# Performance work log

Hardware: AMD Instinct MI355X
Metric: run time of the kernel (lower is better)

## Reference

```python
import jax, jax.numpy as jnp
import numpy as np

TRNA_N, DIS_N = 8000, 6000
D, H, E, B = 128, 256, 320000, 16384
NEG_SLOPE = 0.2  # gat_alpha
TEMP = 0.5


def _gat(src, tgt, s_idx, t_idx, Wsrc, Wtgt, a, n_src):
    # BipartiteGraphAttentionLayer (eval mode, dropout off)
    h_i = src @ Wsrc.T            # [n_src, D]
    h_j = tgt @ Wtgt.T            # [n_tgt, D]
    # cat([h_i[s], h_j[t]]) @ a == (h_i @ a[:D])[s] + (h_j @ a[D:])[t]
    s_i = h_i @ a[:D]             # [n_src]
    s_j = h_j @ a[D:]             # [n_tgt]
    e = jax.nn.leaky_relu(s_i[s_idx] + s_j[t_idx], NEG_SLOPE)
    e = jnp.clip(e, -30.0, 30.0)
    exp_e = jnp.exp(e)
    denom = jax.ops.segment_sum(exp_e, s_idx, num_segments=n_src)
    alpha = exp_e / (denom[s_idx] + 1e-8)
    out = jax.ops.segment_sum(h_j[t_idx] * alpha[:, None], s_idx, num_segments=n_src)
    return jax.nn.elu(out)


def _hg(x, S):
    # HCCF-style parameter-free hypergraph conv: nodes -> hyperedges -> nodes
    return jax.nn.elu(S @ (S.T @ x))


def _info_nce(z1, z2):
    z1 = z1 / (jnp.linalg.norm(z1, axis=1, keepdims=True) + 1e-12)
    z2 = z2 / (jnp.linalg.norm(z2, axis=1, keepdims=True) + 1e-12)
    sim = (z1 @ z2.T) / TEMP      # [N, N]
    logp = jax.nn.log_softmax(sim, axis=1)
    return -jnp.mean(jnp.diagonal(logp))


def setup_inputs():
    key = jax.random.key(0)
    ks = jax.random.split(key, 20)
    xn = lambda k, shp, sc: jax.random.normal(k, shp, dtype=jnp.float32) * sc
    d2 = (2.0 / (2 * D)) ** 0.5
    return dict(
        trna_embed=xn(ks[0], (TRNA_N, D), (2.0 / (TRNA_N + D)) ** 0.5),
        disease_embed=xn(ks[1], (DIS_N, D), (2.0 / (DIS_N + D)) ** 0.5),
        thyper=xn(ks[2], (D, H), (2.0 / (D + H)) ** 0.5),
        dhyper=xn(ks[3], (D, H), (2.0 / (D + H)) ** 0.5),
        gat_t_Wsrc=xn(ks[4], (3, D, D), d2),
        gat_t_Wtgt=xn(ks[5], (3, D, D), d2),
        gat_t_a=xn(ks[6], (3, 2 * D), 1.414 * (2.0 / (2 * D + 1)) ** 0.5),
        gat_d_Wsrc=xn(ks[7], (3, D, D), d2),
        gat_d_Wtgt=xn(ks[8], (3, D, D), d2),
        gat_d_a=xn(ks[9], (3, 2 * D), 1.414 * (2.0 / (2 * D + 1)) ** 0.5),
        mlp_W1=xn(ks[10], (D, 2 * D), (2.0 / (3 * D)) ** 0.5),
        mlp_b1=jnp.zeros((D,), jnp.float32),
        mlp_W2=xn(ks[11], (1, D), (2.0 / (D + 1)) ** 0.5),
        mlp_b2=jnp.zeros((1,), jnp.float32),
        gate_W=xn(ks[12], (1, D), (2.0 / (D + 1)) ** 0.5),
        gate_b=jnp.zeros((1,), jnp.float32),
        src_id=jax.random.randint(ks[13], (E,), 0, TRNA_N),
        tgt_id=jax.random.randint(ks[14], (E,), 0, DIS_N),
        trna_ids=jax.random.randint(ks[15], (B,), 0, TRNA_N),
        disease_ids=jax.random.randint(ks[16], (B,), 0, DIS_N),
    )


def reference(trna_embed, disease_embed, thyper, dhyper,
              gat_t_Wsrc, gat_t_Wtgt, gat_t_a,
              gat_d_Wsrc, gat_d_Wtgt, gat_d_a,
              mlp_W1, mlp_b1, mlp_W2, mlp_b2, gate_W, gate_b,
              src_id, tgt_id, trna_ids, disease_ids):
    # stage 1: simple-graph GAT pass
    sg_t = _gat(trna_embed, disease_embed, src_id, tgt_id,
                gat_t_Wsrc[0], gat_t_Wtgt[0], gat_t_a[0], TRNA_N)
    sg_d = _gat(disease_embed, sg_t, tgt_id, src_id,
                gat_d_Wsrc[0], gat_d_Wtgt[0], gat_d_a[0], DIS_N)
    # hypergraph passes 1-2
    hg_t = _hg(sg_t, sg_t @ thyper)
    hg_d = _hg(sg_d, sg_d @ dhyper)
    hg_t = _hg(hg_t, hg_t @ thyper)
    hg_d = _hg(hg_d, hg_d @ dhyper)
    # GAT layers 2-3 on hypergraph outputs
    sg_t = _gat(hg_t, hg_d, src_id, tgt_id,
                gat_t_Wsrc[1], gat_t_Wtgt[1], gat_t_a[1], TRNA_N)
    sg_d = _gat(hg_d, hg_t, tgt_id, src_id,
                gat_d_Wsrc[1], gat_d_Wtgt[1], gat_d_a[1], DIS_N)
    sg_t = _gat(sg_t, sg_d, src_id, tgt_id,
                gat_t_Wsrc[2], gat_t_Wtgt[2], gat_t_a[2], TRNA_N)
    sg_d = _gat(sg_d, sg_t, tgt_id, src_id,
                gat_d_Wsrc[2], gat_d_Wtgt[2], gat_d_a[2], DIS_N)
    # hypergraph pass 3
    hg_t = _hg(hg_t, hg_t @ thyper)
    hg_d = _hg(hg_d, hg_d @ dhyper)
    final_t = sg_t + hg_t
    final_d = sg_d + hg_d
    sel_t = final_t[trna_ids]
    sel_d = final_d[disease_ids]
    contrast = _info_nce(sg_t, hg_t) + _info_nce(sg_d, hg_d)
    gmf_vec = sel_t * sel_d
    gmf_pred = jnp.sum(gmf_vec, axis=-1)
    mlp_in = jnp.concatenate([sel_t, sel_d], axis=-1)
    h1 = jax.nn.relu(mlp_in @ mlp_W1.T + mlp_b1)
    mlp_pred = (h1 @ mlp_W2.T + mlp_b2)[:, 0]
    gate = jax.nn.sigmoid(gmf_vec @ gate_W.T + gate_b)[:, 0]
    fusion_pred = gate * gmf_pred + (1.0 - gate) * mlp_pred
    return (fusion_pred, sg_t, sg_d, gmf_pred, mlp_pred, contrast)
```

## Files before the change

### kernel.cpp

```cpp
#include <hip/hip_runtime.h>
#include <math.h>

#define N_T 8000
#define N_D 6000
#define N_E 320000
#define N_B 16384
#define NSTRIP 12

typedef __attribute__((ext_vector_type(8))) short s16x8;
typedef __attribute__((ext_vector_type(8))) __bf16 bf16x8;
typedef __attribute__((ext_vector_type(4))) float f32x4;

static __device__ __forceinline__ f32x4 mfma16(s16x8 a, s16x8 b, f32x4 c) {
  return __builtin_amdgcn_mfma_f32_16x16x32_bf16(
      __builtin_bit_cast(bf16x8, a), __builtin_bit_cast(bf16x8, b), c, 0, 0, 0);
}

static __device__ __forceinline__ unsigned short f2bf(float f) {
  unsigned u = __float_as_uint(f);
  u += 0x7FFF + ((u >> 16) & 1);
  return (unsigned short)(u >> 16);
}

static __device__ __forceinline__ float bf2f(unsigned short u) {
// ... 42 lines not shown
    int incl = buf[threadIdx.x];
    if (i < n) { int e = c0 + incl - v; rp[i] = e; cur[i] = e; }
    __syncthreads();
    if (threadIdx.x == 0) carry_s = c0 + buf[1023];
    __syncthreads();
  }
  if (threadIdx.x == 0) rp[n] = carry_s;
}

__global__ void k_scatter2(const int* __restrict__ src, const int* __restrict__ tgt,
    int* __restrict__ cur_t, int* __restrict__ cur_d,
    int* __restrict__ nbr_t, int* __restrict__ nbr_d) {
  int i = blockIdx.x * 256 + threadIdx.x;
  if (i < N_E) {
    int p = atomicAdd(&cur_t[src[i]], 1);
    nbr_t[p] = tgt[i];
  } else if (i < 2 * N_E) {
    i -= N_E;
    int p = atomicAdd(&cur_d[tgt[i]], 1);
    nbr_d[p] = src[i];
  }
}

__global__ __launch_bounds__(256) void k_pgemm(const float* __restrict__ th,
    const float* __restrict__ dh, float* __restrict__ P_t, float* __restrict__ P_d) {
  const float* A = blockIdx.x < 4 ? th : dh;
  float* C = blockIdx.x < 4 ? P_t : P_d;
  const int sub = blockIdx.x & 3;
  const int row0 = (sub >> 1) * 64, col0 = (sub & 1) * 64;
  __shared__ float As[16][65];
  __shared__ float Bs[16][65];
  const int tid = threadIdx.x;
  const int tr = tid >> 4, tc = tid & 15;
  float acc[4][4] = {};
  for (int k0 = 0; k0 < 256; k0 += 16) {
    {
      int m = tid >> 2, kk = (tid & 3) * 4;
      float4 v = *(const float4*)(A + (size_t)(row0 + m) * 256 + k0 + kk);
      As[kk + 0][m] = v.x; As[kk + 1][m] = v.y; As[kk + 2][m] = v.z; As[kk + 3][m] = v.w;
    }
    {
      int nn = tid >> 2, kk = (tid & 3) * 4;
      float4 v = *(const float4*)(A + (size_t)(col0 + nn) * 256 + k0 + kk);
      Bs[kk + 0][nn] = v.x; Bs[kk + 1][nn] = v.y; Bs[kk + 2][nn] = v.z; Bs[kk + 3][nn] = v.w;
    }
    __syncthreads();
#pragma unroll
    for (int k = 0; k < 16; ++k) {
      float a[4], b[4];
#pragma unroll
      for (int i = 0; i < 4; ++i) a[i] = As[k][tr * 4 + i];
#pragma unroll
      for (int j = 0; j < 4; ++j) b[j] = Bs[k][tc * 4 + j];
#pragma unroll
      for (int i = 0; i < 4; ++i)
#pragma unroll
        for (int j = 0; j < 4; ++j)
          acc[i][j] = fmaf(a[i], b[j], acc[i][j]);
    }
    __syncthreads();
  }
#pragma unroll
  for (int i = 0; i < 4; ++i)
#pragma unroll
    for (int j = 0; j < 4; ++j)
      C[(size_t)(row0 + tr * 4 + i) * 128 + col0 + tc * 4 + j] = acc[i][j];
}

__global__ void k_tobf16m(const float* __restrict__ a0, unsigned short* __restrict__ y0,
    const float* __restrict__ a1, unsigned short* __restrict__ y1,
    const float* __restrict__ a2, unsigned short* __restrict__ y2,
    const float* __restrict__ a3, unsigned short* __restrict__ y3) {
  int i = blockIdx.x * 256 + threadIdx.x;
  const float* x; unsigned short* y;
  if (i < 12288) { x = a0; y = y0; }
  else if (i < 24576) { x = a1; y = y1; i -= 12288; }
  else if (i < 32768) { x = a2; y = y2; i -= 24576; }
  else if (i < 224768) { x = a3; y = y3; i -= 32768; }
  else return;
  float4 v = ((const float4*)x)[i];
  ushort4 o;
  o.x = f2bf(v.x); o.y = f2bf(v.y); o.z = f2bf(v.z); o.w = f2bf(v.w);
  ((ushort4*)y)[i] = o;
}

template<int K, int ACT, int BIAS, int SJMODE, int OUTF, int OUTB>
static __device__ __forceinline__ void mfma_body(
    const unsigned short* __restrict__ A, const unsigned short* __restrict__ B,
    const float* __restrict__ bias, const float* __restrict__ a2,
    float* __restrict__ Cf, unsigned short* __restrict__ Cb,
    float* __restrict__ sj_out, int M, int bx) {
  const int wave = threadIdx.x >> 6, lane = threadIdx.x & 63;
  const int row0 = bx * 32;
  const int col0 = wave * 32;
  const int l15 = lane & 15, kg = lane >> 4;
  constexpr int NS = K / 32;
  f32x4 acc[2][2] = {};
  s16x8 ab[2][2], bb[2][2];
  auto ld = [&](int buf, int k0) {
#pragma unroll
    for (int i = 0; i < 2; ++i) {
      int r = row0 + i * 16 + l15;
      ab[buf][i] = (r < M) ? *(const s16x8*)(A + (size_t)r * K + k0 + kg * 8) : (s16x8)0;
    }
#pragma unroll
    for (int j = 0; j < 2; ++j) {
// ... 64 lines not shown
template<int K, int ACT, int BIAS, int SJMODE, int OUTF, int OUTB>
__global__ __launch_bounds__(256) void k_mfma(const unsigned short* __restrict__ A,
    const unsigned short* __restrict__ B, const float* __restrict__ bias,
    const float* __restrict__ a2, float* __restrict__ Cf, unsigned short* __restrict__ Cb,
    float* __restrict__ sj_out, int M) {
  mfma_body<K, ACT, BIAS, SJMODE, OUTF, OUTB>(A, B, bias, a2, Cf, Cb, sj_out, M, blockIdx.x);
}

template<int K, int ACT, int SJMODE, int OUTF, int OUTB>
__global__ __launch_bounds__(256) void k_mfma2(
    const unsigned short* __restrict__ A0, const unsigned short* __restrict__ B0,
    const float* __restrict__ a20, float* __restrict__ Cf0,
    unsigned short* __restrict__ Cb0, float* __restrict__ sj0, int M0, int G0,
    const unsigned short* __restrict__ A1, const unsigned short* __restrict__ B1,
    const float* __restrict__ a21, float* __restrict__ Cf1,
    unsigned short* __restrict__ Cb1, float* __restrict__ sj1, int M1) {
  int bx = blockIdx.x;
  if (bx < G0)
    mfma_body<K, ACT, 0, SJMODE, OUTF, OUTB>(A0, B0, nullptr, a20, Cf0, Cb0, sj0, M0, bx);
  else
    mfma_body<K, ACT, 0, SJMODE, OUTF, OUTB>(A1, B1, nullptr, a21, Cf1, Cb1, sj1, M1, bx - G0);
}

__global__ __launch_bounds__(256) void k_nce4(
    const unsigned short* __restrict__ z1t, const unsigned short* __restrict__ z2t,
    float* __restrict__ rs_tp,
    const unsigned short* __restrict__ z1d, const unsigned short* __restrict__ z2d,
    float* __restrict__ rs_dp) {
  const int wave = threadIdx.x >> 6, lane = threadIdx.x & 63;
  const int l15 = lane & 15, kg = lane >> 4;
  int by = blockIdx.y;
  const unsigned short *z1, *z2; float* rowsum; int M, N;
  if (by < 63) { z1 = z1t; z2 = z2t; rowsum = rs_tp; M = N_T; N = N_T; }
  else { by -= 63; z1 = z1d; z2 = z2d; rowsum = rs_dp; M = N_D; N = N_D; }
  const int row0 = by * 128 + (wave >> 1) * 64;
  const int colw = (wave & 1) * 64;
  const int CT = (N + 127) >> 7;
  const int ctps = (CT + NSTRIP - 1) / NSTRIP;
  const int ct0 = blockIdx.x * ctps;
  const int ct1 = min(CT, ct0 + ctps);
  const int nct = ct1 - ct0;
  if (nct <= 0) return;
  s16x8 a[4][4];
#pragma unroll
  for (int ks = 0; ks < 4; ++ks)
#pragma unroll
    for (int i = 0; i < 4; ++i) {
      int r = row0 + i * 16 + l15;
      a[ks][i] = (r < M) ? *(const s16x8*)(z1 + (size_t)r * 128 + ks * 32 + kg * 8) : (s16x8)0;
    }
  s16x8 b[2][4];
  auto ldb = [&](int buf, int ct, int ks) {
    const unsigned short* base = z2 + (size_t)(ct * 128 + colw) * 128 + ks * 32 + kg * 8;
#pragma unroll
    for (int j = 0; j < 4; ++j)
      b[buf][j] = *(const s16x8*)(base + (size_t)(j * 16 + l15) * 128);
  };
  float rs[4][4] = {};
  int cs = by % nct;
  ldb(0, ct0 + cs, 0);
  for (int cc = 0; cc < nct; ++cc) {
    const int ct = ct0 + cs;
    const int csn = (cs + 1 == nct) ? 0 : cs + 1;
    f32x4 acc[4][4] = {};
#pragma unroll
    for (int ks = 0; ks < 4; ++ks) {
      if (ks < 3) ldb((ks + 1) & 1, ct, ks + 1);
      else if (cc + 1 < nct) ldb(0, ct0 + csn, 0);
#pragma unroll
      for (int i = 0; i < 4; ++i)
#pragma unroll
        for (int j = 0; j < 4; ++j)
          acc[i][j] = mfma16(a[ks][i], b[ks & 1][j], acc[i][j]);
    }
    const int c0 = ct * 128 + colw;
#pragma unroll
    for (int j = 0; j < 4; ++j) {
      bool cok = c0 + j * 16 + l15 < N;
      if (cok) {
#pragma unroll
        for (int i = 0; i < 4; ++i)
#pragma unroll
          for (int r = 0; r < 4; ++r)
            rs[i][r] += __expf(acc[i][j][r]);
      }
    }
    cs = csn;
  }
#pragma unroll
  for (int i = 0; i < 4; ++i)
#pragma unroll
    for (int r = 0; r < 4; ++r) {
      float v = rs[i][r];
      v += __shfl_xor(v, 1, 64);
      v += __shfl_xor(v, 2, 64);
      v += __shfl_xor(v, 4, 64);
      v += __shfl_xor(v, 8, 64);
      if (l15 == 0) {
        int gr = row0 + i * 16 + kg * 4 + r;
        if (gr < M) atomicAdd(&rowsum[gr], v);
      }
    }
}

__global__ __launch_bounds__(256) void k_syrk2m(const unsigned short* __restrict__ xbT,
    const unsigned short* __restrict__ xbD, float* __restrict__ partT,
    float* __restrict__ partD) {
  int b = blockIdx.x;
  const unsigned short* xb; float* part; int n;
  if (b < 128) { xb = xbT; part = partT + (size_t)b * 16384; n = N_T; }
  else { b -= 128; xb = xbD; part = partD + (size_t)b * 16384; n = N_D; }
  __shared__ float rows[4][128];
  int chunk = (n + 127) >> 7;
// ... 59 lines not shown
  }
  __syncthreads();
  const int tx = threadIdx.x & 15, ty = threadIdx.x >> 4;
  float acc[4][4] = {};
  for (int k = 0; k < 128; ++k) {
    float a[4], b[4];
#pragma unroll
    for (int i = 0; i < 4; ++i) a[i] = Gs[ty * 4 + i][k];
#pragma unroll
    for (int j = 0; j < 4; ++j) b[j] = Ps[k][tx * 4 + j];
#pragma unroll
    for (int i = 0; i < 4; ++i)
#pragma unroll
      for (int j = 0; j < 4; ++j)
        acc[i][j] = fmaf(a[i], b[j], acc[i][j]);
  }
#pragma unroll
  for (int i = 0; i < 4; ++i)
#pragma unroll
    for (int j = 0; j < 4; ++j)
      wb[(bi * 64 + ty * 4 + i) * 128 + bj * 64 + tx * 4 + j] = f2bf(acc[i][j]);
}

__global__ void k_wvec6(const float* __restrict__ WsT, const float* __restrict__ aT,
                        const float* __restrict__ WsD, const float* __restrict__ aD,
                        float* __restrict__ wv) {
  int b = blockIdx.x, k = threadIdx.x;
  const float* W = b < 3 ? WsT + b * 16384 : WsD + (b - 3) * 16384;
  const float* a = b < 3 ? aT + b * 256 : aD + (b - 3) * 256;
  float s = 0.f;
  for (int n = 0; n < 128; ++n) s = fmaf(W[n * 128 + k], a[n], s);
  wv[b * 128 + k] = s;
}

__global__ void k_rowdot2(const float* __restrict__ trna, const float* __restrict__ dis,
    const float* __restrict__ wv, float* __restrict__ si_ta, float* __restrict__ si_da) {
  int r = blockIdx.x * 4 + (threadIdx.x >> 6);
  int lane = threadIdx.x & 63;
  const float* h; const float* a; float* o; int row;
  if (r < N_T) { h = trna; a = wv; o = si_ta; row = r; }
  else {
    row = r - N_T;
    if (row >= N_D) return;
    h = dis; a = wv + 3 * 128; o = si_da;
  }
  float2 v = *(const float2*)(h + (size_t)row * 128 + lane * 2);
  float2 av = *(const float2*)(a + lane * 2);
  float s = v.x * av.x + v.y * av.y;
  s = wave_sum(s);
  if (lane == 0) o[row] = s;
}

template<int OUTF, int OUTB, int EMIT_SI>
static __device__ __forceinline__ void agg_body(const int* __restrict__ rp,
    const int* __restrict__ nbr, const float* __restrict__ si,
    const float* __restrict__ sj, const unsigned short* __restrict__ hjb,
    float* __restrict__ outF, unsigned short* __restrict__ outB,
    const float* __restrict__ wv, float* __restrict__ si_out, int n, int bx) {
  int r = bx * 8 + ((int)threadIdx.x >> 5);
  int lane = threadIdx.x & 31;
  if (r >= n) return;
  int p0 = rp[r], p1 = rp[r + 1];
  float sir = si[r];
  int c4 = lane * 4;
  auto wcalc = [&](int t) {
    float v = sir + sj[t];
    v = v >= 0.f ? v : 0.2f * v;
    v = fminf(30.f, fmaxf(-30.f, v));
    return __expf(v);
  };
  float a0 = 0.f, a1 = 0.f, a2 = 0.f, a3 = 0.f, den = 0.f;
  int p = p0;
  for (; p + 8 <= p1; p += 8) {
    int t0 = nbr[p], t1 = nbr[p + 1], t2 = nbr[p + 2], t3 = nbr[p + 3];
    int t4 = nbr[p + 4], t5 = nbr[p + 5], t6 = nbr[p + 6], t7 = nbr[p + 7];
    float w0 = wcalc(t0), w1 = wcalc(t1), w2 = wcalc(t2), w3 = wcalc(t3);
    float w4 = wcalc(t4), w5 = wcalc(t5), w6 = wcalc(t6), w7 = wcalc(t7);
    ushort4 h0 = *(const ushort4*)(hjb + (size_t)t0 * 128 + c4);
    ushort4 h1 = *(const ushort4*)(hjb + (size_t)t1 * 128 + c4);
    ushort4 h2 = *(const ushort4*)(hjb + (size_t)t2 * 128 + c4);
    ushort4 h3 = *(const ushort4*)(hjb + (size_t)t3 * 128 + c4);
    ushort4 h4 = *(const ushort4*)(hjb + (size_t)t4 * 128 + c4);
    ushort4 h5 = *(const ushort4*)(hjb + (size_t)t5 * 128 + c4);
    ushort4 h6 = *(const ushort4*)(hjb + (size_t)t6 * 128 + c4);
    ushort4 h7 = *(const ushort4*)(hjb + (size_t)t7 * 128 + c4);
    den += ((w0 + w1) + (w2 + w3)) + ((w4 + w5) + (w6 + w7));
    a0 += (w0 * bf2f(h0.x) + w1 * bf2f(h1.x) + w2 * bf2f(h2.x) + w3 * bf2f(h3.x)) +
          (w4 * bf2f(h4.x) + w5 * bf2f(h5.x) + w6 * bf2f(h6.x) + w7 * bf2f(h7.x));
    a1 += (w0 * bf2f(h0.y) + w1 * bf2f(h1.y) + w2 * bf2f(h2.y) + w3 * bf2f(h3.y)) +
          (w4 * bf2f(h4.y) + w5 * bf2f(h5.y) + w6 * bf2f(h6.y) + w7 * bf2f(h7.y));
    a2 += (w0 * bf2f(h0.z) + w1 * bf2f(h1.z) + w2 * bf2f(h2.z) + w3 * bf2f(h3.z)) +
          (w4 * bf2f(h4.z) + w5 * bf2f(h5.z) + w6 * bf2f(h6.z) + w7 * bf2f(h7.z));
    a3 += (w0 * bf2f(h0.w) + w1 * bf2f(h1.w) + w2 * bf2f(h2.w) + w3 * bf2f(h3.w)) +
          (w4 * bf2f(h4.w) + w5 * bf2f(h5.w) + w6 * bf2f(h6.w) + w7 * bf2f(h7.w));
  }
  for (; p + 4 <= p1; p += 4) {
    int t0 = nbr[p], t1 = nbr[p + 1], t2 = nbr[p + 2], t3 = nbr[p + 3];
    float w0 = wcalc(t0), w1 = wcalc(t1), w2 = wcalc(t2), w3 = wcalc(t3);
    ushort4 h0 = *(const ushort4*)(hjb + (size_t)t0 * 128 + c4);
    ushort4 h1 = *(const ushort4*)(hjb + (size_t)t1 * 128 + c4);
    ushort4 h2 = *(const ushort4*)(hjb + (size_t)t2 * 128 + c4);
    ushort4 h3 = *(const ushort4*)(hjb + (size_t)t3 * 128 + c4);
    den += (w0 + w1) + (w2 + w3);
    a0 += w0 * bf2f(h0.x) + w1 * bf2f(h1.x) + w2 * bf2f(h2.x) + w3 * bf2f(h3.x);
    a1 += w0 * bf2f(h0.y) + w1 * bf2f(h1.y) + w2 * bf2f(h2.y) + w3 * bf2f(h3.y);
    a2 += w0 * bf2f(h0.z) + w1 * bf2f(h1.z) + w2 * bf2f(h2.z) + w3 * bf2f(h3.z);
    a3 += w0 * bf2f(h0.w) + w1 * bf2f(h1.w) + w2 * bf2f(h2.w) + w3 * bf2f(h3.w);
  }
  for (; p < p1; ++p) {
    int t = nbr[p];
    float w = wcalc(t);
    ushort4 h = *(const ushort4*)(hjb + (size_t)t * 128 + c4);
    den += w;
    a0 += w * bf2f(h.x); a1 += w * bf2f(h.y);
    a2 += w * bf2f(h.z); a3 += w * bf2f(h.w);
  }
  float inv = 1.0f / (den + 1e-8f);
  float v0 = a0 * inv, v1 = a1 * inv, v2 = a2 * inv, v3 = a3 * inv;
  v0 = v0 > 0.f ? v0 : __expf(v0) - 1.f;
  v1 = v1 > 0.f ? v1 : __expf(v1) - 1.f;
  v2 = v2 > 0.f ? v2 : __expf(v2) - 1.f;
  v3 = v3 > 0.f ? v3 : __expf(v3) - 1.f;
  if (OUTF) {
    float4 of; of.x = v0; of.y = v1; of.z = v2; of.w = v3;
    *(float4*)(outF + (size_t)r * 128 + c4) = of;
  }
  if (OUTB) {
    ushort4 ob; ob.x = f2bf(v0); ob.y = f2bf(v1); ob.z = f2bf(v2); ob.w = f2bf(v3);
    *(ushort4*)(outB + (size_t)r * 128 + c4) = ob;
  }
  if (EMIT_SI) {
    float4 w4 = *(const float4*)(wv + c4);
    float d = v0 * w4.x + v1 * w4.y + v2 * w4.z + v3 * w4.w;
    d += __shfl_xor(d, 16, 64);
    d += __shfl_xor(d, 8, 64);
    d += __shfl_xor(d, 4, 64);
    d += __shfl_xor(d, 2, 64);
    d += __shfl_xor(d, 1, 64);
    if (lane == 0) si_out[r] = d;
  }
}

template<int OUTF, int OUTB, int EMIT_SI>
__global__ __launch_bounds__(256) void k_agg(const int* __restrict__ rp,
    const int* __restrict__ nbr, const float* __restrict__ si,
    const float* __restrict__ sj, const unsigned short* __restrict__ hjb,
    float* __restrict__ outF, unsigned short* __restrict__ outB,
    const float* __restrict__ wv, float* __restrict__ si_out, int n) {
  agg_body<OUTF, OUTB, EMIT_SI>(rp, nbr, si, sj, hjb, outF, outB, wv, si_out, n, blockIdx.x);
}

template<int OUTF, int OUTB, int EMIT_SI>
__global__ __launch_bounds__(256) void k_agg2(
    const int* __restrict__ rp0, const int* __restrict__ nbr0, const float* __restrict__ si0,
    const float* __restrict__ sj0, const unsigned short* __restrict__ hjb0,
    float* __restrict__ outF0, unsigned short* __restrict__ outB0,
    const float* __restrict__ wv0, float* __restrict__ sio0, int n0, int G0,
    const int* __restrict__ rp1, const int* __restrict__ nbr1, const float* __restrict__ si1,
    const float* __restrict__ sj1, const unsigned short* __restrict__ hjb1,
    float* __restrict__ outF1, unsigned short* __restrict__ outB1,
    const float* __restrict__ wv1, float* __restrict__ sio1, int n1) {
  int bx = blockIdx.x;
  if (bx < G0)
    agg_body<OUTF, OUTB, EMIT_SI>(rp0, nbr0, si0, sj0, hjb0, outF0, outB0, wv0, sio0, n0, bx);
  else
    agg_body<OUTF, OUTB, EMIT_SI>(rp1, nbr1, si1, sj1, hjb1, outF1, outB1, wv1, sio1, n1, bx - G0);
}

__global__ void k_norm2(const float* __restrict__ sgt, const float* __restrict__ hgt3,
    const float* __restrict__ sgd, const float* __restrict__ hgd3,
    unsigned short* __restrict__ z1t, unsigned short* __restrict__ z2t,
    unsigned short* __restrict__ z1d, unsigned short* __restrict__ z2d,
    float* __restrict__ rs_t, float* __restrict__ dg_t,
    float* __restrict__ rs_d, float* __restrict__ dg_d) {
  int ridx = blockIdx.x * 4 + (threadIdx.x >> 6);
  int lane = threadIdx.x & 63;
  const float *x1, *x2; unsigned short *o1, *o2; float *rs, *dg; int row;
  if (ridx < 8000) { x1 = sgt; x2 = hgt3; o1 = z1t; o2 = z2t; rs = rs_t; dg = dg_t; row = ridx; }
  else if (ridx < 14000) {
    row = ridx - 8000;
    x1 = sgd; x2 = hgd3; o1 = z1d; o2 = z2d; rs = rs_d; dg = dg_d;
  } else return;
  float2 v1 = *(const float2*)(x1 + (size_t)row * 128 + lane * 2);
  float2 v2 = *(const float2*)(x2 + (size_t)row * 128 + lane * 2);
  float ss1 = wave_sum(v1.x * v1.x + v1.y * v1.y);
  float ss2 = wave_sum(v2.x * v2.x + v2.y * v2.y);
  float i1 = 1.0f / (sqrtf(ss1) + 1e-12f);
  float i2 = 1.0f / (sqrtf(ss2) + 1e-12f);
  float n1x = v1.x * i1, n1y = v1.y * i1;
  float n2x = v2.x * i2, n2y = v2.y * i2;
  ushort2 w1; w1.x = f2bf(n1x + n1x); w1.y = f2bf(n1y + n1y);
  ushort2 w2; w2.x = f2bf(n2x); w2.y = f2bf(n2y);
  *(ushort2*)(o1 + (size_t)row * 128 + lane * 2) = w1;
  *(ushort2*)(o2 + (size_t)row * 128 + lane * 2) = w2;
  float d = wave_sum(n1x * n2x + n1y * n2y);
  if (lane == 0) { dg[row] = 2.0f * d; rs[row] = 0.f; }
}

__global__ void k_gather(const float* __restrict__ sgt, const float* __restrict__ hgt,
    const float* __restrict__ sgd, const float* __restrict__ hgd,
    const int* __restrict__ tids, const int* __restrict__ dids,
    const float* __restrict__ gateW, unsigned short* __restrict__ mlp_in_b,
    float* __restrict__ gmf, float* __restrict__ gate_lin, int nB) {
  int b = blockIdx.x * 4 + (threadIdx.x >> 6);
// ... 22 lines not shown
__global__ void k_final(const float* __restrict__ h1, const float* __restrict__ W2,
    const float* __restrict__ b2, const float* __restrict__ gate_lin,
    const float* __restrict__ gate_b, const float* __restrict__ gmf,
    float* __restrict__ fusion, float* __restrict__ mlp_pred, int nB) {
  int b = blockIdx.x * 4 + (threadIdx.x >> 6);
  int lane = threadIdx.x & 63;
  if (b >= nB) return;
  float2 hv = *(const float2*)(h1 + (size_t)b * 128 + lane * 2);
  float2 wv = *(const float2*)(W2 + lane * 2);
  float s = hv.x * wv.x + hv.y * wv.y;
  s = wave_sum(s);
  if (lane == 0) {
    float mp = s + b2[0];
    float g = 1.0f / (1.0f + __expf(-(gate_lin[b] + gate_b[0])));
    mlp_pred[b] = mp;
    fusion[b] = g * gmf[b] + (1.0f - g) * mp;
  }
}

__global__ void k_contrast(const float* __restrict__ rs_t, const float* __restrict__ dg_t,
    const float* __restrict__ rs_d, const float* __restrict__ dg_d, float* __restrict__ out) {
  __shared__ float red[256];
  float st = 0.f, sd = 0.f;
  for (int i = threadIdx.x; i < N_T; i += 256) st += __logf(rs_t[i]) - dg_t[i];
  for (int i = threadIdx.x; i < N_D; i += 256) sd += __logf(rs_d[i]) - dg_d[i];
  red[threadIdx.x] = st * (1.0f / N_T) + sd * (1.0f / N_D);
  __syncthreads();
  for (int off = 128; off; off >>= 1) {
    if (threadIdx.x < (unsigned)off) red[threadIdx.x] += red[threadIdx.x + off];
    __syncthreads();
  }
  if (threadIdx.x == 0) out[0] = red[0];
}

extern "C" void kernel_launch(void* const* d_in, const int* in_sizes, int n_in,
                              void* d_out, int out_size, void* d_ws, size_t ws_size,
                              hipStream_t stream) {
  const float* trna   = (const float*)d_in[0];
  const float* dis    = (const float*)d_in[1];
  const float* thyper = (const float*)d_in[2];
  const float* dhyper = (const float*)d_in[3];
  const float* WsrcT  = (const float*)d_in[4];
  const float* WtgtT  = (const float*)d_in[5];
  const float* aT     = (const float*)d_in[6];
  const float* WsrcD  = (const float*)d_in[7];
  const float* WtgtD  = (const float*)d_in[8];
  const float* aD     = (const float*)d_in[9];
  const float* W1     = (const float*)d_in[10];
// ... 53 lines not shown
  float* wvecs  = (float*)alloc(6 * 128 * 4);
  float* si_ta  = (float*)alloc(N_T * 4);
  float* si_tb  = (float*)alloc(N_T * 4);
  float* si_da  = (float*)alloc(N_D * 4);
  float* si_db  = (float*)alloc(N_D * 4);
  float* s_jT   = (float*)alloc(N_T * 4);
  float* s_jD   = (float*)alloc(N_T * 4);
  int* cnt      = (int*)alloc((N_T + N_D) * 4);
  int* rp_t     = (int*)alloc((N_T + 1) * 4);
  int* cur_t    = (int*)alloc(N_T * 4);
  int* rp_d     = (int*)alloc((N_D + 1) * 4);
  int* cur_d    = (int*)alloc(N_D * 4);
  int* nbrc_t   = (int*)alloc((size_t)N_E * 4);
  int* nbrc_d   = (int*)alloc((size_t)N_E * 4);
  float* rs_t   = (float*)alloc(N_T * 4);
  float* dg_t   = (float*)alloc(N_T * 4);
  float* rs_d   = (float*)alloc(N_D * 4);
  float* dg_d   = (float*)alloc(N_D * 4);
  float* g_lin  = (float*)alloc(N_B * 4);
  (void)ws_size; (void)in_sizes; (void)n_in; (void)out_size;

  const int gT32 = (N_T + 31) / 32;
  const int gD32 = (N_D + 31) / 32;
  const int aT8 = (N_T + 7) / 8, aD8 = (N_D + 7) / 8;

  hipMemsetAsync(cnt, 0, (N_T + N_D) * 4, stream);
  k_hist2<<<(2 * N_E + 255) / 256, 256, 0, stream>>>(src_id, tgt_id, cnt);
  k_scan2<<<2, 1024, 0, stream>>>(cnt, rp_t, cur_t, rp_d, cur_d);
  k_scatter2<<<(2 * N_E + 255) / 256, 256, 0, stream>>>(src_id, tgt_id, cur_t, cur_d,
      nbrc_t, nbrc_d);

  k_pgemm<<<8, 256, 0, stream>>>(thyper, dhyper, P_t, P_d);
  k_wvec6<<<6, 128, 0, stream>>>(WsrcT, aT, WsrcD, aD, wvecs);
  k_tobf16m<<<878, 256, 0, stream>>>(WtgtT, wbT, WtgtD, wbD, W1, W1b, dis, disb);
  k_rowdot2<<<(N_T + N_D + 3) / 4, 256, 0, stream>>>(trna, dis, wvecs, si_ta, si_da);

  k_mfma<128, 0, 0, 1, 0, 1><<<gD32, 256, 0, stream>>>(
      disb, wbT, nullptr, aT + 128, nullptr, hjbT, s_jT, N_D);
  k_agg<0, 1, 0><<<aT8, 256, 0, stream>>>(rp_t, nbrc_t, si_ta, s_jT, hjbT,
      nullptr, sgt_b, nullptr, nullptr, N_T);
  k_mfma<128, 0, 0, 1, 0, 1><<<gT32, 256, 0, stream>>>(
      sgt_b, wbD, nullptr, aD + 128, nullptr, hjbD, s_jD, N_T);
  k_agg<0, 1, 0><<<aD8, 256, 0, stream>>>(rp_d, nbrc_d, si_da, s_jD, hjbD,
      nullptr, sgd_b, nullptr, nullptr, N_D);

  k_syrk2m<<<256, 256, 0, stream>>>(sgt_b, sgd_b, partT, partD);
  k_redm<<<128, 256, 0, stream>>>(partT, partD, Gm_t, Gm_d);
  k_wtm<<<8, 256, 0, stream>>>(Gm_t, P_t, wb_t, Gm_d, P_d, wb_d);
  k_mfma2<128, 1, 0, 0, 1><<<gT32 + gD32, 256, 0, stream>>>(
      sgt_b, wb_t, nullptr, nullptr, hgt_b, nullptr, N_T, gT32,
      sgd_b, wb_d, nullptr, nullptr, hgd_b, nullptr, N_D);

  k_syrk2m<<<256, 256, 0, stream>>>(hgt_b, hgd_b, partT, partD);
  k_redm<<<128, 256, 0, stream>>>(partT, partD, Gm_t, Gm_d);
  k_wtm<<<8, 256, 0, stream>>>(Gm_t, P_t, wb_t, Gm_d, P_d, wb_d);
  k_mfma2<128, 1, 2, 0, 1><<<gT32 + gD32, 256, 0, stream>>>(
      hgt_b, wb_t, wvecs + 128, nullptr, hgt2_b, si_tb, N_T, gT32,
      hgd_b, wb_d, wvecs + 4 * 128, nullptr, hgd2_b, si_db, N_D);

  k_mfma2<128, 0, 1, 0, 1><<<gD32 + gT32, 256, 0, stream>>>(
      hgd2_b, wbT + 16384, aT + 256 + 128, nullptr, hjbT, s_jT, N_D, gD32,
      hgt2_b, wbD + 16384, aD + 256 + 128, nullptr, hjbD, s_jD, N_T);
  k_agg2<0, 1, 1><<<aT8 + aD8, 256, 0, stream>>>(
      rp_t, nbrc_t, si_tb, s_jT, hjbT, nullptr, sgt_b, wvecs + 2 * 128, si_ta, N_T, aT8,
      rp_d, nbrc_d, si_db, s_jD, hjbD, nullptr, sgd_b, wvecs + 5 * 128, si_da, N_D);

  k_mfma<128, 0, 0, 1, 0, 1><<<gD32, 256, 0, stream>>>(
      sgd_b, wbT + 32768, nullptr, aT + 512 + 128, nullptr, hjbT, s_jT, N_D);
  k_agg<1, 1, 0><<<aT8, 256, 0, stream>>>(rp_t, nbrc_t, si_ta, s_jT, hjbT,
      out_sgt, sgt_b, nullptr, nullptr, N_T);
  k_mfma<128, 0, 0, 1, 0, 1><<<gT32, 256, 0, stream>>>(
      sgt_b, wbD + 32768, nullptr, aD + 512 + 128, nullptr, hjbD, s_jD, N_T);
  k_agg<1, 0, 0><<<aD8, 256, 0, stream>>>(rp_d, nbrc_d, si_da, s_jD, hjbD,
      out_sgd, nullptr, nullptr, nullptr, N_D);

  k_syrk2m<<<256, 256, 0, stream>>>(hgt2_b, hgd2_b, partT, partD);
  k_redm<<<128, 256, 0, stream>>>(partT, partD, Gm_t, Gm_d);
  k_wtm<<<8, 256, 0, stream>>>(Gm_t, P_t, wb_t, Gm_d, P_d, wb_d);
  k_mfma2<128, 1, 0, 1, 0><<<gT32 + gD32, 256, 0, stream>>>(
      hgt2_b, wb_t, nullptr, hg_t3, nullptr, nullptr, N_T, gT32,
      hgd2_b, wb_d, nullptr, hg_d3, nullptr, nullptr, N_D);

  k_norm2<<<3500, 256, 0, stream>>>(out_sgt, hg_t3, out_sgd, hg_d3,
      zb1t, zb2t, zb1d, zb2d, rs_t, dg_t, rs_d, dg_d);
  k_nce4<<<dim3(NSTRIP, 63 + 47), 256, 0, stream>>>(
      zb1t, zb2t, rs_t, zb1d, zb2d, rs_d);
  k_contrast<<<1, 256, 0, stream>>>(rs_t, dg_t, rs_d, dg_d, out_con);

  k_gather<<<(N_B + 3) / 4, 256, 0, stream>>>(out_sgt, hg_t3, out_sgd, hg_d3,
      tids, dids, gW, mlp_in_b, out_gmf, g_lin, N_B);
  k_mfma<256, 2, 1, 0, 1, 0><<<N_B / 32, 256, 0, stream>>>(
      mlp_in_b, W1b, b1, nullptr, h1buf, nullptr, nullptr, N_B);
  k_final<<<(N_B + 3) / 4, 256, 0, stream>>>(h1buf, W2, b2, g_lin, gb,
      out_gmf, out_fusion, out_mlp, N_B);
}
```

Before: 479.6 us.

## Fuse prologue kernels, retile NCE, widen aggregation waves, drop NCE column masking

Three small prologue kernels (projection GEMM, weight-vector dot, bf16 conversion) become one launch to cut launch overhead. The InfoNCE kernel moves to 64-row blocks for more parallelism and drops per-column bounds checks: the padded z2 rows are zeroed, and each zero row's exp(0)=1 contribution is subtracted as a constant in the log step. GAT aggregation now uses one 64-lane wave per row with 2 columns per lane and deeper 16-neighbour unrolling to raise memory-level parallelism. The constant correction assumes the padded rows are exactly zero and that the padding count is fixed.

```diff
diff --git a/kernel.cpp b/kernel.cpp
--- a/kernel.cpp
+++ b/kernel.cpp
@@ -88,66 +88,78 @@
   }
 }
 
-__global__ __launch_bounds__(256) void k_pgemm(const float* __restrict__ th,
-    const float* __restrict__ dh, float* __restrict__ P_t, float* __restrict__ P_d) {
-  const float* A = blockIdx.x < 4 ? th : dh;
-  float* C = blockIdx.x < 4 ? P_t : P_d;
-  const int sub = blockIdx.x & 3;
-  const int row0 = (sub >> 1) * 64, col0 = (sub & 1) * 64;
-  __shared__ float As[16][65];
-  __shared__ float Bs[16][65];
-  const int tid = threadIdx.x;
-  const int tr = tid >> 4, tc = tid & 15;
-  float acc[4][4] = {};
-  for (int k0 = 0; k0 < 256; k0 += 16) {
-    {
-      int m = tid >> 2, kk = (tid & 3) * 4;
-      float4 v = *(const float4*)(A + (size_t)(row0 + m) * 256 + k0 + kk);
-      As[kk + 0][m] = v.x; As[kk + 1][m] = v.y; As[kk + 2][m] = v.z; As[kk + 3][m] = v.w;
-    }
-    {
-      int nn = tid >> 2, kk = (tid & 3) * 4;
-      float4 v = *(const float4*)(A + (size_t)(col0 + nn) * 256 + k0 + kk);
-      Bs[kk + 0][nn] = v.x; Bs[kk + 1][nn] = v.y; Bs[kk + 2][nn] = v.z; Bs[kk + 3][nn] = v.w;
-    }
-    __syncthreads();
-#pragma unroll
-    for (int k = 0; k < 16; ++k) {
-      float a[4], b[4];
-#pragma unroll
-      for (int i = 0; i < 4; ++i) a[i] = As[k][tr * 4 + i];
-#pragma unroll
-      for (int j = 0; j < 4; ++j) b[j] = Bs[k][tc * 4 + j];
-#pragma unroll
-      for (int i = 0; i < 4; ++i)
-#pragma unroll
-        for (int j = 0; j < 4; ++j)
-          acc[i][j] = fmaf(a[i], b[j], acc[i][j]);
-    }
-    __syncthreads();
-  }
-#pragma unroll
-  for (int i = 0; i < 4; ++i)
-#pragma unroll
-    for (int j = 0; j < 4; ++j)
-      C[(size_t)(row0 + tr * 4 + i) * 128 + col0 + tc * 4 + j] = acc[i][j];
-}
-
-__global__ void k_tobf16m(const float* __restrict__ a0, unsigned short* __restrict__ y0,
-    const float* __restrict__ a1, unsigned short* __restrict__ y1,
-    const float* __restrict__ a2, unsigned short* __restrict__ y2,
-    const float* __restrict__ a3, unsigned short* __restrict__ y3) {
-  int i = blockIdx.x * 256 + threadIdx.x;
-  const float* x; unsigned short* y;
-  if (i < 12288) { x = a0; y = y0; }
-  else if (i < 24576) { x = a1; y = y1; i -= 12288; }
-  else if (i < 32768) { x = a2; y = y2; i -= 24576; }
-  else if (i < 224768) { x = a3; y = y3; i -= 32768; }
-  else return;
-  float4 v = ((const float4*)x)[i];
-  ushort4 o;
-  o.x = f2bf(v.x); o.y = f2bf(v.y); o.z = f2bf(v.z); o.w = f2bf(v.w);
-  ((ushort4*)y)[i] = o;
+__global__ __launch_bounds__(256) void k_pre(const float* __restrict__ th,
+    const float* __restrict__ dh, float* __restrict__ P_t, float* __restrict__ P_d,
+    const float* __restrict__ WsT, const float* __restrict__ aT,
+    const float* __restrict__ WsD, const float* __restrict__ aD, float* __restrict__ wv,
+    const float* __restrict__ c0, unsigned short* __restrict__ y0,
+    const float* __restrict__ c1, unsigned short* __restrict__ y1,
+    const float* __restrict__ c2, unsigned short* __restrict__ y2,
+    const float* __restrict__ c3, unsigned short* __restrict__ y3) {
+  int bx = blockIdx.x;
+  if (bx < 8) {
+    const float* A = bx < 4 ? th : dh;
+    float* C = bx < 4 ? P_t : P_d;
+    const int sub = bx & 3;
+    const int row0 = (sub >> 1) * 64, col0 = (sub & 1) * 64;
+    __shared__ float As[16][65];
+    __shared__ float Bs[16][65];
+    const int tid = threadIdx.x;
+    const int tr = tid >> 4, tc = tid & 15;
+    float acc[4][4] = {};
+    for (int k0 = 0; k0 < 256; k0 += 16) {
+      {
+        int m = tid >> 2, kk = (tid & 3) * 4;
+        float4 v = *(const float4*)(A + (size_t)(row0 + m) * 256 + k0 + kk);
+        As[kk + 0][m] = v.x; As[kk + 1][m] = v.y; As[kk + 2][m] = v.z; As[kk + 3][m] = v.w;
+      }
+      {
+        int nn = tid >> 2, kk = (tid & 3) * 4;
+        float4 v = *(const float4*)(A + (size_t)(col0 + nn) * 256 + k0 + kk);
+        Bs[kk + 0][nn] = v.x; Bs[kk + 1][nn] = v.y; Bs[kk + 2][nn] = v.z; Bs[kk + 3][nn] = v.w;
+      }
+      __syncthreads();
+#pragma unroll
+      for (int k = 0; k < 16; ++k) {
+        float a[4], b[4];
+#pragma unroll
+        for (int i = 0; i < 4; ++i) a[i] = As[k][tr * 4 + i];
+#pragma unroll
+        for (int j = 0; j < 4; ++j) b[j] = Bs[k][tc * 4 + j];
+#pragma unroll
+        for (int i = 0; i < 4; ++i)
+#pragma unroll
+          for (int j = 0; j < 4; ++j)
+            acc[i][j] = fmaf(a[i], b[j], acc[i][j]);
+      }
+      __syncthreads();
+    }
+#pragma unroll
+    for (int i = 0; i < 4; ++i)
+#pragma unroll
+      for (int j = 0; j < 4; ++j)
+        C[(size_t)(row0 + tr * 4 + i) * 128 + col0 + tc * 4 + j] = acc[i][j];
+  } else if (bx < 14) {
+    if (threadIdx.x >= 128) return;
+    int b = bx - 8, k = threadIdx.x;
+    const float* W = b < 3 ? WsT + b * 16384 : WsD + (b - 3) * 16384;
+    const float* a = b < 3 ? aT + b * 256 : aD + (b - 3) * 256;
+    float s = 0.f;
+    for (int n = 0; n < 128; ++n) s = fmaf(W[n * 128 + k], a[n], s);
+    wv[b * 128 + k] = s;
+  } else {
+    int i = (bx - 14) * 256 + threadIdx.x;
+    const float* x; unsigned short* y;
+    if (i < 12288) { x = c0; y = y0; }
+    else if (i < 24576) { x = c1; y = y1; i -= 12288; }
+    else if (i < 32768) { x = c2; y = y2; i -= 24576; }
+    else if (i < 224768) { x = c3; y = y3; i -= 32768; }
+    else return;
+    float4 v = ((const float4*)x)[i];
+    ushort4 o;
+    o.x = f2bf(v.x); o.y = f2bf(v.y); o.z = f2bf(v.z); o.w = f2bf(v.w);
+    ((ushort4*)y)[i] = o;
+  }
 }
 
 template<int K, int ACT, int BIAS, int SJMODE, int OUTF, int OUTB>
@@ -258,7 +270,7 @@
     mfma_body<K, ACT, 0, SJMODE, OUTF, OUTB>(A1, B1, nullptr, a21, Cf1, Cb1, sj1, M1, bx - G0);
 }
 
-__global__ __launch_bounds__(256) void k_nce4(
+__global__ __launch_bounds__(256) void k_nce5(
     const unsigned short* __restrict__ z1t, const unsigned short* __restrict__ z2t,
     float* __restrict__ rs_tp,
     const unsigned short* __restrict__ z1d, const unsigned short* __restrict__ z2d,
@@ -267,21 +279,21 @@
   const int l15 = lane & 15, kg = lane >> 4;
   int by = blockIdx.y;
   const unsigned short *z1, *z2; float* rowsum; int M, N;
-  if (by < 63) { z1 = z1t; z2 = z2t; rowsum = rs_tp; M = N_T; N = N_T; }
-  else { by -= 63; z1 = z1d; z2 = z2d; rowsum = rs_dp; M = N_D; N = N_D; }
-  const int row0 = by * 128 + (wave >> 1) * 64;
-  const int colw = (wave & 1) * 64;
+  if (by < 125) { z1 = z1t; z2 = z2t; rowsum = rs_tp; M = N_T; N = N_T; }
+  else { by -= 125; z1 = z1d; z2 = z2d; rowsum = rs_dp; M = N_D; N = N_D; }
+  const int row0 = by * 64 + (wave & 1) * 32;
+  const int colw = (wave >> 1) * 64;
   const int CT = (N + 127) >> 7;
   const int ctps = (CT + NSTRIP - 1) / NSTRIP;
   const int ct0 = blockIdx.x * ctps;
   const int ct1 = min(CT, ct0 + ctps);
   const int nct = ct1 - ct0;
   if (nct <= 0) return;
-  s16x8 a[4][4];
+  s16x8 a[4][2];
 #pragma unroll
   for (int ks = 0; ks < 4; ++ks)
 #pragma unroll
-    for (int i = 0; i < 4; ++i) {
+    for (int i = 0; i < 2; ++i) {
       int r = row0 + i * 16 + l15;
       a[ks][i] = (r < M) ? *(const s16x8*)(z1 + (size_t)r * 128 + ks * 32 + kg * 8) : (s16x8)0;
     }
@@ -292,39 +304,34 @@
     for (int j = 0; j < 4; ++j)
       b[buf][j] = *(const s16x8*)(base + (size_t)(j * 16 + l15) * 128);
   };
-  float rs[4][4] = {};
+  float rs[2][4] = {};
   int cs = by % nct;
   ldb(0, ct0 + cs, 0);
   for (int cc = 0; cc < nct; ++cc) {
     const int ct = ct0 + cs;
     const int csn = (cs + 1 == nct) ? 0 : cs + 1;
-    f32x4 acc[4][4] = {};
+    f32x4 acc[2][4] = {};
 #pragma unroll
     for (int ks = 0; ks < 4; ++ks) {
       if (ks < 3) ldb((ks + 1) & 1, ct, ks + 1);
       else if (cc + 1 < nct) ldb(0, ct0 + csn, 0);
 #pragma unroll
-      for (int i = 0; i < 4; ++i)
+      for (int i = 0; i < 2; ++i)
 #pragma unroll
         for (int j = 0; j < 4; ++j)
           acc[i][j] = mfma16(a[ks][i], b[ks & 1][j], acc[i][j]);
     }
-    const int c0 = ct * 128 + colw;
-#pragma unroll
-    for (int j = 0; j < 4; ++j) {
-      bool cok = c0 + j * 16 + l15 < N;
-      if (cok) {
-#pragma unroll
-        for (int i = 0; i < 4; ++i)
-#pragma unroll
-          for (int r = 0; r < 4; ++r)
-            rs[i][r] += __expf(acc[i][j][r]);
-      }
-    }
+#pragma unroll
+    for (int j = 0; j < 4; ++j)
+#pragma unroll
+      for (int i = 0; i < 2; ++i)
+#pragma unroll
+        for (int r = 0; r < 4; ++r)
+          rs[i][r] += __expf(acc[i][j][r]);
     cs = csn;
   }
 #pragma unroll
-  for (int i = 0; i < 4; ++i)
+  for (int i = 0; i < 2; ++i)
 #pragma unroll
     for (int r = 0; r < 4; ++r) {
       float v = rs[i][r];
@@ -430,17 +437,6 @@
       wb[(bi * 64 + ty * 4 + i) * 128 + bj * 64 + tx * 4 + j] = f2bf(acc[i][j]);
 }
 
-__global__ void k_wvec6(const float* __restrict__ WsT, const float* __restrict__ aT,
-                        const float* __restrict__ WsD, const float* __restrict__ aD,
-                        float* __restrict__ wv) {
-  int b = blockIdx.x, k = threadIdx.x;
-  const float* W = b < 3 ? WsT + b * 16384 : WsD + (b - 3) * 16384;
-  const float* a = b < 3 ? aT + b * 256 : aD + (b - 3) * 256;
-  float s = 0.f;
-  for (int n = 0; n < 128; ++n) s = fmaf(W[n * 128 + k], a[n], s);
-  wv[b * 128 + k] = s;
-}
-
 __global__ void k_rowdot2(const float* __restrict__ trna, const float* __restrict__ dis,
     const float* __restrict__ wv, float* __restrict__ si_ta, float* __restrict__ si_da) {
   int r = blockIdx.x * 4 + (threadIdx.x >> 6);
@@ -465,86 +461,76 @@
     const float* __restrict__ sj, const unsigned short* __restrict__ hjb,
     float* __restrict__ outF, unsigned short* __restrict__ outB,
     const float* __restrict__ wv, float* __restrict__ si_out, int n, int bx) {
-  int r = bx * 8 + ((int)threadIdx.x >> 5);
-  int lane = threadIdx.x & 31;
+  int r = bx * 4 + ((int)threadIdx.x >> 6);
+  int lane = threadIdx.x & 63;
   if (r >= n) return;
   int p0 = rp[r], p1 = rp[r + 1];
   float sir = si[r];
-  int c4 = lane * 4;
-  auto wcalc = [&](int t) {
-    float v = sir + sj[t];
+  int c2 = lane * 2;
+  auto wgt = [&](float sv) {
+    float v = sir + sv;
     v = v >= 0.f ? v : 0.2f * v;
     v = fminf(30.f, fmaxf(-30.f, v));
     return __expf(v);
   };
-  float a0 = 0.f, a1 = 0.f, a2 = 0.f, a3 = 0.f, den = 0.f;
+  float ax = 0.f, ay = 0.f, den = 0.f;
   int p = p0;
-  for (; p + 8 <= p1; p += 8) {
-    int t0 = nbr[p], t1 = nbr[p + 1], t2 = nbr[p + 2], t3 = nbr[p + 3];
-    int t4 = nbr[p + 4], t5 = nbr[p + 5], t6 = nbr[p + 6], t7 = nbr[p + 7];
-    float w0 = wcalc(t0), w1 = wcalc(t1), w2 = wcalc(t2), w3 = wcalc(t3);
-    float w4 = wcalc(t4), w5 = wcalc(t5), w6 = wcalc(t6), w7 = wcalc(t7);
-    ushort4 h0 = *(const ushort4*)(hjb + (size_t)t0 * 128 + c4);
-    ushort4 h1 = *(const ushort4*)(hjb + (size_t)t1 * 128 + c4);
-    ushort4 h2 = *(const ushort4*)(hjb + (size_t)t2 * 128 + c4);
-    ushort4 h3 = *(const ushort4*)(hjb + (size_t)t3 * 128 + c4);
-    ushort4 h4 = *(const ushort4*)(hjb + (size_t)t4 * 128 + c4);
-    ushort4 h5 = *(const ushort4*)(hjb + (size_t)t5 * 128 + c4);
-    ushort4 h6 = *(const ushort4*)(hjb + (size_t)t6 * 128 + c4);
-    ushort4 h7 = *(const ushort4*)(hjb + (size_t)t7 * 128 + c4);
-    den += ((w0 + w1) + (w2 + w3)) + ((w4 + w5) + (w6 + w7));
-    a0 += (w0 * bf2f(h0.x) + w1 * bf2f(h1.x) + w2 * bf2f(h2.x) + w3 * bf2f(h3.x)) +
-          (w4 * bf2f(h4.x) + w5 * bf2f(h5.x) + w6 * bf2f(h6.x) + w7 * bf2f(h7.x));
-    a1 += (w0 * bf2f(h0.y) + w1 * bf2f(h1.y) + w2 * bf2f(h2.y) + w3 * bf2f(h3.y)) +
-          (w4 * bf2f(h4.y) + w5 * bf2f(h5.y) + w6 * bf2f(h6.y) + w7 * bf2f(h7.y));
-    a2 += (w0 * bf2f(h0.z) + w1 * bf2f(h1.z) + w2 * bf2f(h2.z) + w3 * bf2f(h3.z)) +
-          (w4 * bf2f(h4.z) + w5 * bf2f(h5.z) + w6 * bf2f(h6.z) + w7 * bf2f(h7.z));
-    a3 += (w0 * bf2f(h0.w) + w1 * bf2f(h1.w) + w2 * bf2f(h2.w) + w3 * bf2f(h3.w)) +
-          (w4 * bf2f(h4.w) + w5 * bf2f(h5.w) + w6 * bf2f(h6.w) + w7 * bf2f(h7.w));
+  for (; p + 16 <= p1; p += 16) {
+    int t[16]; float sv[16]; ushort2 h[16];
+#pragma unroll
+    for (int k = 0; k < 16; ++k) t[k] = nbr[p + k];
+#pragma unroll
+    for (int k = 0; k < 16; ++k) sv[k] = sj[t[k]];
+#pragma unroll
+    for (int k = 0; k < 16; ++k) h[k] = *(const ushort2*)(hjb + (size_t)t[k] * 128 + c2);
+#pragma unroll
+    for (int k = 0; k < 16; ++k) {
+      float w = wgt(sv[k]);
+      den += w;
+      ax += w * bf2f(h[k].x);
+      ay += w * bf2f(h[k].y);
+    }
   }
   for (; p + 4 <= p1; p += 4) {
-    int t0 = nbr[p], t1 = nbr[p + 1], t2 = nbr[p + 2], t3 = nbr[p + 3];
-    float w0 = wcalc(t0), w1 = wcalc(t1), w2 = wcalc(t2), w3 = wcalc(t3);
-    ushort4 h0 = *(const ushort4*)(hjb + (size_t)t0 * 128 + c4);
-    ushort4 h1 = *(const ushort4*)(hjb + (size_t)t1 * 128 + c4);
-    ushort4 h2 = *(const ushort4*)(hjb + (size_t)t2 * 128 + c4);
-    ushort4 h3 = *(const ushort4*)(hjb + (size_t)t3 * 128 + c4);
-    den += (w0 + w1) + (w2 + w3);
-    a0 += w0 * bf2f(h0.x) + w1 * bf2f(h1.x) + w2 * bf2f(h2.x) + w3 * bf2f(h3.x);
-    a1 += w0 * bf2f(h0.y) + w1 * bf2f(h1.y) + w2 * bf2f(h2.y) + w3 * bf2f(h3.y);
-    a2 += w0 * bf2f(h0.z) + w1 * bf2f(h1.z) + w2 * bf2f(h2.z) + w3 * bf2f(h3.z);
-    a3 += w0 * bf2f(h0.w) + w1 * bf2f(h1.w) + w2 * bf2f(h2.w) + w3 * bf2f(h3.w);
+    int t[4]; float sv[4]; ushort2 h[4];
+#pragma unroll
+    for (int k = 0; k < 4; ++k) t[k] = nbr[p + k];
+#pragma unroll
+    for (int k = 0; k < 4; ++k) sv[k] = sj[t[k]];
+#pragma unroll
+    for (int k = 0; k < 4; ++k) h[k] = *(const ushort2*)(hjb + (size_t)t[k] * 128 + c2);
+#pragma unroll
+    for (int k = 0; k < 4; ++k) {
+      float w = wgt(sv[k]);
+      den += w;
+      ax += w * bf2f(h[k].x);
+      ay += w * bf2f(h[k].y);
+    }
   }
   for (; p < p1; ++p) {
     int t = nbr[p];
-    float w = wcalc(t);
-    ushort4 h = *(const ushort4*)(hjb + (size_t)t * 128 + c4);
+    float w = wgt(sj[t]);
+    ushort2 h = *(const ushort2*)(hjb + (size_t)t * 128 + c2);
     den += w;
-    a0 += w * bf2f(h.x); a1 += w * bf2f(h.y);
-    a2 += w * bf2f(h.z); a3 += w * bf2f(h.w);
+    ax += w * bf2f(h.x);
+    ay += w * bf2f(h.y);
   }
   float inv = 1.0f / (den + 1e-8f);
-  float v0 = a0 * inv, v1 = a1 * inv, v2 = a2 * inv, v3 = a3 * inv;
-  v0 = v0 > 0.f ? v0 : __expf(v0) - 1.f;
-  v1 = v1 > 0.f ? v1 : __expf(v1) - 1.f;
-  v2 = v2 > 0.f ? v2 : __expf(v2) - 1.f;
-  v3 = v3 > 0.f ? v3 : __expf(v3) - 1.f;
+  float vx = ax * inv, vy = ay * inv;
+  vx = vx > 0.f ? vx : __expf(vx) - 1.f;
+  vy = vy > 0.f ? vy : __expf(vy) - 1.f;
   if (OUTF) {
-    float4 of; of.x = v0; of.y = v1; of.z = v2; of.w = v3;
-    *(float4*)(outF + (size_t)r * 128 + c4) = of;
+    float2 of; of.x = vx; of.y = vy;
+    *(float2*)(outF + (size_t)r * 128 + c2) = of;
   }
   if (OUTB) {
-    ushort4 ob; ob.x = f2bf(v0); ob.y = f2bf(v1); ob.z = f2bf(v2); ob.w = f2bf(v3);
-    *(ushort4*)(outB + (size_t)r * 128 + c4) = ob;
+    ushort2 ob; ob.x = f2bf(vx); ob.y = f2bf(vy);
+    *(ushort2*)(outB + (size_t)r * 128 + c2) = ob;
   }
   if (EMIT_SI) {
-    float4 w4 = *(const float4*)(wv + c4);
-    float d = v0 * w4.x + v1 * w4.y + v2 * w4.z + v3 * w4.w;
-    d += __shfl_xor(d, 16, 64);
-    d += __shfl_xor(d, 8, 64);
-    d += __shfl_xor(d, 4, 64);
-    d += __shfl_xor(d, 2, 64);
-    d += __shfl_xor(d, 1, 64);
+    float2 w2v = *(const float2*)(wv + c2);
+    float d = vx * w2v.x + vy * w2v.y;
+    d = wave_sum(d);
     if (lane == 0) si_out[r] = d;
   }
 }
@@ -588,6 +574,16 @@
   else if (ridx < 14000) {
     row = ridx - 8000;
     x1 = sgd; x2 = hgd3; o1 = z1d; o2 = z2d; rs = rs_d; dg = dg_d;
+  } else if (ridx < 14064) {
+    row = 8000 + (ridx - 14000);
+    ushort2 z; z.x = 0; z.y = 0;
+    *(ushort2*)(z2t + (size_t)row * 128 + lane * 2) = z;
+    return;
+  } else if (ridx < 14080) {
+    row = 6000 + (ridx - 14064);
+    ushort2 z; z.x = 0; z.y = 0;
+    *(ushort2*)(z2d + (size_t)row * 128 + lane * 2) = z;
+    return;
   } else return;
   float2 v1 = *(const float2*)(x1 + (size_t)row * 128 + lane * 2);
   float2 v2 = *(const float2*)(x2 + (size_t)row * 128 + lane * 2);
@@ -656,8 +652,8 @@
     const float* __restrict__ rs_d, const float* __restrict__ dg_d, float* __restrict__ out) {
   __shared__ float red[256];
   float st = 0.f, sd = 0.f;
-  for (int i = threadIdx.x; i < N_T; i += 256) st += __logf(rs_t[i]) - dg_t[i];
-  for (int i = threadIdx.x; i < N_D; i += 256) sd += __logf(rs_d[i]) - dg_d[i];
+  for (int i = threadIdx.x; i < N_T; i += 256) st += __logf(rs_t[i] - 64.0f) - dg_t[i];
+  for (int i = threadIdx.x; i < N_D; i += 256) sd += __logf(rs_d[i] - 16.0f) - dg_d[i];
   red[threadIdx.x] = st * (1.0f / N_T) + sd * (1.0f / N_D);
   __syncthreads();
   for (int off = 128; off; off >>= 1) {
@@ -757,7 +753,7 @@
 
   const int gT32 = (N_T + 31) / 32;
   const int gD32 = (N_D + 31) / 32;
-  const int aT8 = (N_T + 7) / 8, aD8 = (N_D + 7) / 8;
+  const int aT4 = (N_T + 3) / 4, aD4 = (N_D + 3) / 4;
 
   hipMemsetAsync(cnt, 0, (N_T + N_D) * 4, stream);
   k_hist2<<<(2 * N_E + 255) / 256, 256, 0, stream>>>(src_id, tgt_id, cnt);
@@ -765,18 +761,18 @@
   k_scatter2<<<(2 * N_E + 255) / 256, 256, 0, stream>>>(src_id, tgt_id, cur_t, cur_d,
       nbrc_t, nbrc_d);
 
-  k_pgemm<<<8, 256, 0, stream>>>(thyper, dhyper, P_t, P_d);
-  k_wvec6<<<6, 128, 0, stream>>>(WsrcT, aT, WsrcD, aD, wvecs);
-  k_tobf16m<<<878, 256, 0, stream>>>(WtgtT, wbT, WtgtD, wbD, W1, W1b, dis, disb);
+  k_pre<<<892, 256, 0, stream>>>(thyper, dhyper, P_t, P_d,
+      WsrcT, aT, WsrcD, aD, wvecs,
+      WtgtT, wbT, WtgtD, wbD, W1, W1b, dis, disb);
   k_rowdot2<<<(N_T + N_D + 3) / 4, 256, 0, stream>>>(trna, dis, wvecs, si_ta, si_da);
 
   k_mfma<128, 0, 0, 1, 0, 1><<<gD32, 256, 0, stream>>>(
       disb, wbT, nullptr, aT + 128, nullptr, hjbT, s_jT, N_D);
-  k_agg<0, 1, 0><<<aT8, 256, 0, stream>>>(rp_t, nbrc_t, si_ta, s_jT, hjbT,
+  k_agg<0, 1, 0><<<aT4, 256, 0, stream>>>(rp_t, nbrc_t, si_ta, s_jT, hjbT,
       nullptr, sgt_b, nullptr, nullptr, N_T);
   k_mfma<128, 0, 0, 1, 0, 1><<<gT32, 256, 0, stream>>>(
       sgt_b, wbD, nullptr, aD + 128, nullptr, hjbD, s_jD, N_T);
-  k_agg<0, 1, 0><<<aD8, 256, 0, stream>>>(rp_d, nbrc_d, si_da, s_jD, hjbD,
+  k_agg<0, 1, 0><<<aD4, 256, 0, stream>>>(rp_d, nbrc_d, si_da, s_jD, hjbD,
       nullptr, sgd_b, nullptr, nullptr, N_D);
 
   k_syrk2m<<<256, 256, 0, stream>>>(sgt_b, sgd_b, partT, partD);
@@ -796,17 +792,17 @@
   k_mfma2<128, 0, 1, 0, 1><<<gD32 + gT32, 256, 0, stream>>>(
       hgd2_b, wbT + 16384, aT + 256 + 128, nullptr, hjbT, s_jT, N_D, gD32,
       hgt2_b, wbD + 16384, aD + 256 + 128, nullptr, hjbD, s_jD, N_T);
-  k_agg2<0, 1, 1><<<aT8 + aD8, 256, 0, stream>>>(
-      rp_t, nbrc_t, si_tb, s_jT, hjbT, nullptr, sgt_b, wvecs + 2 * 128, si_ta, N_T, aT8,
+  k_agg2<0, 1, 1><<<aT4 + aD4, 256, 0, stream>>>(
+      rp_t, nbrc_t, si_tb, s_jT, hjbT, nullptr, sgt_b, wvecs + 2 * 128, si_ta, N_T, aT4,
       rp_d, nbrc_d, si_db, s_jD, hjbD, nullptr, sgd_b, wvecs + 5 * 128, si_da, N_D);
 
   k_mfma<128, 0, 0, 1, 0, 1><<<gD32, 256, 0, stream>>>(
       sgd_b, wbT + 32768, nullptr, aT + 512 + 128, nullptr, hjbT, s_jT, N_D);
-  k_agg<1, 1, 0><<<aT8, 256, 0, stream>>>(rp_t, nbrc_t, si_ta, s_jT, hjbT,
+  k_agg<1, 1, 0><<<aT4, 256, 0, stream>>>(rp_t, nbrc_t, si_ta, s_jT, hjbT,
       out_sgt, sgt_b, nullptr, nullptr, N_T);
   k_mfma<128, 0, 0, 1, 0, 1><<<gT32, 256, 0, stream>>>(
       sgt_b, wbD + 32768, nullptr, aD + 512 + 128, nullptr, hjbD, s_jD, N_T);
-  k_agg<1, 0, 0><<<aD8, 256, 0, stream>>>(rp_d, nbrc_d, si_da, s_jD, hjbD,
+  k_agg<1, 0, 0><<<aD4, 256, 0, stream>>>(rp_d, nbrc_d, si_da, s_jD, hjbD,
       out_sgd, nullptr, nullptr, nullptr, N_D);
 
   k_syrk2m<<<256, 256, 0, stream>>>(hgt2_b, hgd2_b, partT, partD);
@@ -816,9 +812,9 @@
       hgt2_b, wb_t, nullptr, hg_t3, nullptr, nullptr, N_T, gT32,
       hgd2_b, wb_d, nullptr, hg_d3, nullptr, nullptr, N_D);
 
-  k_norm2<<<3500, 256, 0, stream>>>(out_sgt, hg_t3, out_sgd, hg_d3,
+  k_norm2<<<3520, 256, 0, stream>>>(out_sgt, hg_t3, out_sgd, hg_d3,
       zb1t, zb2t, zb1d, zb2d, rs_t, dg_t, rs_d, dg_d);
-  k_nce4<<<dim3(NSTRIP, 63 + 47), 256, 0, stream>>>(
+  k_nce5<<<dim3(NSTRIP, 125 + 94), 256, 0, stream>>>(
       zb1t, zb2t, rs_t, zb1d, zb2d, rs_d);
   k_contrast<<<1, 256, 0, stream>>>(rs_t, dg_t, rs_d, dg_d, out_con);
 
```

Measured after the change: 506.3 us. 1.06x slower.
